# Kernel tuning notes

Measured on AMD Instinct MI355X. Metric: run time of the kernel, lower is better.

The kernel has to match this reference:

```python
import jax, jax.numpy as jnp
import numpy as np

B, S, H, L = 64, 512, 1024, 5  # batch, seq_len, BiLSTM feature dim (2*512), num fine P labels


def setup_inputs() -> dict:
    key = jax.random.key(0)
    ks = jax.random.split(key, 8)
    feats = jax.random.normal(ks[0], (B, S, H), dtype=jnp.float32)
    labels = jax.random.randint(ks[1], (B, S), 0, L)
    mask = jnp.ones((B, S), dtype=bool)  # CRF requires mask[:, 0] all on
    W_tag = jax.random.normal(ks[2], (H, L), dtype=jnp.float32) * 0.02
    b_tag = jnp.zeros((L,), dtype=jnp.float32)
    start_trans = jax.random.normal(ks[3], (L,), dtype=jnp.float32) * 0.1
    end_trans = jax.random.normal(ks[4], (L,), dtype=jnp.float32) * 0.1
    trans = jax.random.normal(ks[5], (L, L), dtype=jnp.float32) * 0.1
    weights = jax.random.uniform(ks[6], (L,), dtype=jnp.float32, minval=0.5, maxval=1.5)
    return dict(feats=feats, labels=labels, mask=mask, W_tag=W_tag, b_tag=b_tag,
                start_trans=start_trans, end_trans=end_trans, trans=trans, weights=weights)


def reference(feats, labels, mask, W_tag, b_tag, start_trans, end_trans, trans, weights):
    # hidden2tag + relu (as in the torch module: probablity = F.relu(self.hidden2tag(...)))
    emissions = jax.nn.relu(feats @ W_tag + b_tag)  # [B, S, L]
    maskf = mask.astype(emissions.dtype)            # [B, S]

    # ---- weighted CRF negative log-likelihood, reduction='token_mean' ----
    # numerator: gold-path score, per-token emission contributions scaled by class weights
    em_tag = jnp.take_along_axis(emissions, labels[..., None], axis=2)[..., 0]  # [B, S]
    numerator = (start_trans[labels[:, 0]]
                 + jnp.sum(weights[labels] * em_tag * maskf, axis=1)
                 + jnp.sum(trans[labels[:, :-1], labels[:, 1:]] * maskf[:, 1:], axis=1)
                 + end_trans[labels[:, -1]])  # [B]

    # partition function via forward algorithm (scan over time)
    emis_t = emissions[:, 1:].swapaxes(0, 1)  # [S-1, B, L]
    mask_t = mask[:, 1:].T                    # [S-1, B]

    def fwd_step(alpha, x):
        e, m = x  # [B, L], [B]
        new = jax.nn.logsumexp(alpha[:, :, None] + trans[None, :, :], axis=1) + e
        return jnp.where(m[:, None], new, alpha), None

    alpha0 = start_trans[None, :] + emissions[:, 0]  # [B, L]
    alpha, _ = jax.lax.scan(fwd_step, alpha0, (emis_t, mask_t))
    log_z = jax.nn.logsumexp(alpha + end_trans[None, :], axis=1)  # [B]

    loss = -jnp.sum(numerator - log_z) / maskf.sum()

    # ---- Viterbi decode ----
    def vit_step(v, x):
        e, m = x
        scores = v[:, :, None] + trans[None, :, :]  # [B, L_prev, L_cur]
        best = jnp.max(scores, axis=1) + e
        idx = jnp.argmax(scores, axis=1)            # backpointers [B, L]
        return jnp.where(m[:, None], best, v), idx

    v, hist = jax.lax.scan(vit_step, start_trans[None, :] + emissions[:, 0], (emis_t, mask_t))
    last = jnp.argmax(v + end_trans[None, :], axis=1)  # [B] tag at position S-1
    b_idx = jnp.arange(labels.shape[0])

    def back_step(tag, bp):
        prev = bp[b_idx, tag]
        return prev, tag  # emit tag at position t+1

    first, path_rest = jax.lax.scan(back_step, last, hist, reverse=True)  # [B], [S-1, B]
    paths = jnp.concatenate([first[None, :], path_rest], axis=0).T  # [B, S]

    return loss, paths
```

## Files before the change

kernel.cpp:

```cpp
#include <hip/hip_runtime.h>

namespace {

constexpr int kB = 64, kS = 512, kH = 1024, kL = 5;
constexpr int kRows = kB * kS;
constexpr float kNegInf = -1e30f;
constexpr int kChunks = 6;

__device__ inline float rl(float x, int i) {
  return __uint_as_float(__builtin_amdgcn_readlane(__float_as_uint(x), i));
}

__global__ __launch_bounds__(256) void emis_kernel(
    const float* __restrict__ feats, const float* __restrict__ W,
    const float* __restrict__ b_tag, float* __restrict__ emis,
    float* __restrict__ out_loss, int nwaves) {
  if (blockIdx.x == 0 && threadIdx.x == 0) out_loss[0] = 0.0f;

  const int lane = threadIdx.x & 63;
  const int wave = blockIdx.x * (blockDim.x >> 6) + (threadIdx.x >> 6);

  float wreg[4][20];
#pragma unroll
  for (int k0 = 0; k0 < 4; ++k0) {
    const float4* wp =
        reinterpret_cast<const float4*>(W + (k0 * 256 + lane * 4) * kL);
#pragma unroll
    for (int q = 0; q < 5; ++q) {
      float4 w = wp[q];
      wreg[k0][q * 4 + 0] = w.x;
      wreg[k0][q * 4 + 1] = w.y;
      wreg[k0][q * 4 + 2] = w.z;
      wreg[k0][q * 4 + 3] = w.w;
    }
  }

  for (int r = 2 * wave; r < kRows; r += 2 * nwaves) {
    const float4* fa = reinterpret_cast<const float4*>(feats + (size_t)r * kH);
    const float4* fb =
        reinterpret_cast<const float4*>(feats + (size_t)(r + 1) * kH);
    float accA[kL] = {0.f, 0.f, 0.f, 0.f, 0.f};
    float accB[kL] = {0.f, 0.f, 0.f, 0.f, 0.f};
#pragma unroll
    for (int k0 = 0; k0 < 4; ++k0) {
      float4 xa = fa[(k0 << 6) + lane];
      float4 xb = fb[(k0 << 6) + lane];
      const float* wr = wreg[k0];
#pragma unroll
      for (int l = 0; l < kL; ++l) {
        accA[l] = fmaf(xa.x, wr[l], accA[l]);
        accA[l] = fmaf(xa.y, wr[5 + l], accA[l]);
        accA[l] = fmaf(xa.z, wr[10 + l], accA[l]);
        accA[l] = fmaf(xa.w, wr[15 + l], accA[l]);
        accB[l] = fmaf(xb.x, wr[l], accB[l]);
        accB[l] = fmaf(xb.y, wr[5 + l], accB[l]);
        accB[l] = fmaf(xb.z, wr[10 + l], accB[l]);
        accB[l] = fmaf(xb.w, wr[15 + l], accB[l]);
      }
    }
#pragma unroll
    for (int off = 32; off >= 1; off >>= 1)
#pragma unroll
      for (int l = 0; l < kL; ++l) {
        accA[l] += __shfl_xor(accA[l], off, 64);
        accB[l] += __shfl_xor(accB[l], off, 64);
      }
    if (lane < kL) {
      emis[(size_t)r * kL + lane] = fmaxf(accA[lane] + b_tag[lane], 0.0f);
      emis[(size_t)(r + 1) * kL + lane] = fmaxf(accB[lane] + b_tag[lane], 0.0f);
    }
  }
}

__global__ __launch_bounds__(512) void scan_kernel(
    const float* __restrict__ emis, const int* __restrict__ labels,
    const float* __restrict__ start_trans, const float* __restrict__ end_trans,
    const float* __restrict__ trans, const float* __restrict__ weights,
    float* __restrict__ out_loss, float* __restrict__ out_paths) {
  const int b = blockIdx.x;
  const int tid = threadIdx.x;
  const int lane = tid & 63;
  const int wv = tid >> 6;

  __shared__ float e_lds[(kS + 4) * kL];
  __shared__ float v_lds[kS * kL];
  __shared__ float t_lds[25];
  __shared__ unsigned short f_a[kS], f_b[kS];
  __shared__ float M_lds[kChunks * 25];
  __shared__ double num_sh;
  __shared__ int last_sh;

  {
    const float4* src =
        reinterpret_cast<const float4*>(emis + (size_t)b * kS * kL);
    float4* dst = reinterpret_cast<float4*>(e_lds);
    for (int i = tid; i < kS * kL / 4; i += 512) dst[i] = src[i];
    if (tid < 4 * kL) e_lds[kS * kL + tid] = 0.0f;
    if (tid < 25) t_lds[tid] = trans[tid];
  }
  __syncthreads();

  const int j = (lane < kL) ? lane : 0;

  if (wv == 0) {
    const bool act = lane < kL;
    float tf[kL];
#pragma unroll
    for (int i = 0; i < kL; ++i) tf[i] = t_lds[i * kL + j];
    float vd = start_trans[j] + e_lds[j];
    if (act) v_lds[lane] = vd;
    float e0 = e_lds[1 * kL + j], e1 = e_lds[2 * kL + j],
          e2 = e_lds[3 * kL + j], e3 = e_lds[4 * kL + j];
#pragma unroll 4
    for (int t = 1; t < kS; ++t) {
      float en = e_lds[(t + 4) * kL + j];
      float s0 = rl(vd, 0), s1 = rl(vd, 1), s2 = rl(vd, 2), s3 = rl(vd, 3),
            s4 = rl(vd, 4);
      float c0 = s0 + tf[0], c1 = s1 + tf[1], c2 = s2 + tf[2],
            c3 = s3 + tf[3], c4 = s4 + tf[4];
      float m = fmaxf(fmaxf(fmaxf(c0, c1), fmaxf(c2, c3)), c4);
      vd = m + e0;
      if (act) v_lds[t * kL + lane] = vd;
      e0 = e1; e1 = e2; e2 = e3; e3 = en;
    }
    float v0 = rl(vd, 0), v1 = rl(vd, 1), v2 = rl(vd, 2), v3 = rl(vd, 3),
          v4 = rl(vd, 4);
    if (lane == 0) {
      float best = v0 + end_trans[0];
      int last = 0;
      float cc;
      cc = v1 + end_trans[1]; if (cc > best) { best = cc; last = 1; }
      cc = v2 + end_trans[2]; if (cc > best) { best = cc; last = 2; }
      cc = v3 + end_trans[3]; if (cc > best) { best = cc; last = 3; }
      cc = v4 + end_trans[4]; if (cc > best) { best = cc; last = 4; }
      last_sh = last;
    }
  } else if (wv == 1) {
    double num = 0.0;
    for (int t = lane; t < kS; t += 64) {
      int lt = labels[b * kS + t];
      num += (double)weights[lt] * (double)e_lds[t * kL + lt];
      if (t > 0) {
        int lp = labels[b * kS + t - 1];
        num += (double)t_lds[lp * kL + lt];
      }
    }
#pragma unroll
    for (int off = 32; off >= 1; off >>= 1) num += __shfl_xor(num, off, 64);
    if (lane == 0) {
      int l0 = labels[b * kS];
      int lS = labels[b * kS + kS - 1];
      num_sh = num + (double)start_trans[l0] + (double)end_trans[lS];
    }
  } else {
    const int c = wv - 2;
    const int t0 = 1 + 86 * c;
    const int t1 = (t0 + 86 < kS) ? (t0 + 86) : kS;
    const int ci = (lane < 25) ? (lane / 5) : 0;
    const int cj = (lane < 25) ? (lane % 5) : 0;
    float tf[kL];
#pragma unroll
    for (int k = 0; k < kL; ++k) tf[k] = t_lds[k * kL + cj];
    float m = (lane < 25 && ci == cj) ? 0.0f : kNegInf;
    float e_cur = e_lds[t0 * kL + cj];
    for (int t = t0; t < t1; ++t) {
      float e_nxt = (t + 1 < t1) ? e_lds[(t + 1) * kL + cj] : 0.0f;
      float m0 = __shfl(m, ci * 5 + 0, 64), m1 = __shfl(m, ci * 5 + 1, 64),
            m2 = __shfl(m, ci * 5 + 2, 64), m3 = __shfl(m, ci * 5 + 3, 64),
            m4 = __shfl(m, ci * 5 + 4, 64);
      float c0 = m0 + tf[0], c1 = m1 + tf[1], c2 = m2 + tf[2],
            c3 = m3 + tf[3], c4 = m4 + tf[4];
      float mx = fmaxf(fmaxf(fmaxf(c0, c1), fmaxf(c2, c3)), c4);
      float s = __expf(c0 - mx) + __expf(c1 - mx) + __expf(c2 - mx) +
                __expf(c3 - mx) + __expf(c4 - mx);
      m = mx + __logf(s) + e_cur;
      e_cur = e_nxt;
    }
    if (lane < 25) M_lds[c * 25 + lane] = m;
  }
  __syncthreads();

  if (tid < kS - 1) {
    float v0 = v_lds[tid * kL + 0], v1 = v_lds[tid * kL + 1],
          v2 = v_lds[tid * kL + 2], v3 = v_lds[tid * kL + 3],
          v4 = v_lds[tid * kL + 4];
    unsigned int w = 0;
#pragma unroll
    for (int q = 0; q < kL; ++q) {
      float best = v0 + t_lds[0 * kL + q];
      int bi = 0;
      float bb;
      bb = v1 + t_lds[1 * kL + q]; if (bb > best) { best = bb; bi = 1; }
      bb = v2 + t_lds[2 * kL + q]; if (bb > best) { best = bb; bi = 2; }
      bb = v3 + t_lds[3 * kL + q]; if (bb > best) { best = bb; bi = 3; }
      bb = v4 + t_lds[4 * kL + q]; if (bb > best) { best = bb; bi = 4; }
      w |= (unsigned int)bi << (3 * q);
    }
    f_a[tid + 1] = (unsigned short)w;
  }
  __syncthreads();

  unsigned short* src = f_a;
  unsigned short* dst = f_b;
  for (int off = 1; off < kS; off <<= 1) {
    if (tid >= 1) {
      unsigned short v = src[tid];
      if (tid + off < kS) {
        unsigned int a = v, g = src[tid + off], r = 0;
#pragma unroll
        for (int x = 0; x < kL; ++x) {
          unsigned int bx = (g >> (3 * x)) & 7u;
          r |= ((a >> (3 * bx)) & 7u) << (3 * x);
        }
        v = (unsigned short)r;
      }
      dst[tid] = v;
    }
    __syncthreads();
    unsigned short* tmp = src; src = dst; dst = tmp;
  }

  const int last = last_sh;
  if (tid < kS - 1) {
    unsigned short g = src[tid + 1];
    out_paths[(size_t)b * kS + tid] = (float)((g >> (3 * last)) & 7u);
  } else if (tid == kS - 1) {
    out_paths[(size_t)b * kS + tid] = (float)last;
  }

  if (wv == 1) {
    float alpha = start_trans[j] + e_lds[j];
#pragma unroll 1
    for (int c = 0; c < kChunks; ++c) {
      float a0 = __shfl(alpha, 0, 64), a1 = __shfl(alpha, 1, 64),
            a2 = __shfl(alpha, 2, 64), a3 = __shfl(alpha, 3, 64),
            a4 = __shfl(alpha, 4, 64);
      float c0 = a0 + M_lds[c * 25 + 0 + j], c1 = a1 + M_lds[c * 25 + 5 + j],
            c2 = a2 + M_lds[c * 25 + 10 + j], c3 = a3 + M_lds[c * 25 + 15 + j],
            c4 = a4 + M_lds[c * 25 + 20 + j];
      float mx = fmaxf(fmaxf(fmaxf(c0, c1), fmaxf(c2, c3)), c4);
      float s = __expf(c0 - mx) + __expf(c1 - mx) + __expf(c2 - mx) +
                __expf(c3 - mx) + __expf(c4 - mx);
      alpha = mx + __logf(s);
    }
    float aj[kL];
#pragma unroll
    for (int i = 0; i < kL; ++i) aj[i] = __shfl(alpha, i, 64);
    if (lane == 0) {
      float c0 = aj[0] + end_trans[0], c1 = aj[1] + end_trans[1],
            c2 = aj[2] + end_trans[2], c3 = aj[3] + end_trans[3],
            c4 = aj[4] + end_trans[4];
      float mx = fmaxf(fmaxf(fmaxf(c0, c1), fmaxf(c2, c3)), c4);
      float logz =
          mx + __logf(__expf(c0 - mx) + __expf(c1 - mx) + __expf(c2 - mx) +
                      __expf(c3 - mx) + __expf(c4 - mx));
      double term = num_sh - (double)logz;
      atomicAdd(out_loss, (float)(-term / (double)(kB * kS)));
    }
  }
}

}

extern "C" void kernel_launch(void* const* d_in, const int* in_sizes, int n_in,
                              void* d_out, int out_size, void* d_ws,
                              size_t ws_size, hipStream_t stream) {
  const float* feats = (const float*)d_in[0];
  const int* labels = (const int*)d_in[1];
  const float* W_tag = (const float*)d_in[3];
  const float* b_tag = (const float*)d_in[4];
  const float* start_trans = (const float*)d_in[5];
  const float* end_trans = (const float*)d_in[6];
  const float* trans = (const float*)d_in[7];
  const float* weights = (const float*)d_in[8];

  float* emis = (float*)d_ws;
  float* out = (float*)d_out;

  const int blocks = 2048;
  const int nwaves = blocks * 4;
  emis_kernel<<<blocks, 256, 0, stream>>>(feats, W_tag, b_tag, emis, out,
                                          nwaves);
  scan_kernel<<<kB, 512, 0, stream>>>(emis, labels, start_trans, end_trans,
                                      trans, weights, out, out + 1);
}
```

Baseline: 234.3 us.

## Fuse emission GEMV and CRF scan into one kernel with per-batch ready flags

Merges the emission projection and the CRF forward/Viterbi scan into a single launch. The emission blocks are assigned per batch, and each one increments that batch's flag after storing its rows. Scan blocks, placed at the end of the grid, spin on their batch's flag and start as soon as that batch's emissions are ready. This removes the kernel boundary and lets scans overlap the remaining GEMV work, at the cost of two memsets, atomic stores, and a forward-progress dependence on scan blocks being scheduled after the producer blocks.

```diff
diff --git a/kernel.cpp b/kernel.cpp
--- a/kernel.cpp
+++ b/kernel.cpp
@@ -3,39 +3,47 @@
 namespace {
 
 constexpr int kB = 64, kS = 512, kH = 1024, kL = 5;
-constexpr int kRows = kB * kS;
 constexpr float kNegInf = -1e30f;
 constexpr int kChunks = 6;
+constexpr int kEmisBlocks = 2048;
+constexpr int kBlocksPerBatch = 32;
 
 __device__ inline float rl(float x, int i) {
   return __uint_as_float(__builtin_amdgcn_readlane(__float_as_uint(x), i));
 }
 
-__global__ __launch_bounds__(256) void emis_kernel(
+__global__ __launch_bounds__(512) void fused_kernel(
     const float* __restrict__ feats, const float* __restrict__ W,
-    const float* __restrict__ b_tag, float* __restrict__ emis,
-    float* __restrict__ out_loss, int nwaves) {
-  if (blockIdx.x == 0 && threadIdx.x == 0) out_loss[0] = 0.0f;
-
-  const int lane = threadIdx.x & 63;
-  const int wave = blockIdx.x * (blockDim.x >> 6) + (threadIdx.x >> 6);
-
-  float wreg[4][20];
-#pragma unroll
-  for (int k0 = 0; k0 < 4; ++k0) {
-    const float4* wp =
-        reinterpret_cast<const float4*>(W + (k0 * 256 + lane * 4) * kL);
-#pragma unroll
-    for (int q = 0; q < 5; ++q) {
-      float4 w = wp[q];
-      wreg[k0][q * 4 + 0] = w.x;
-      wreg[k0][q * 4 + 1] = w.y;
-      wreg[k0][q * 4 + 2] = w.z;
-      wreg[k0][q * 4 + 3] = w.w;
-    }
-  }
-
-  for (int r = 2 * wave; r < kRows; r += 2 * nwaves) {
+    const float* __restrict__ b_tag, const int* __restrict__ labels,
+    const float* __restrict__ start_trans, const float* __restrict__ end_trans,
+    const float* __restrict__ trans, const float* __restrict__ weights,
+    float* __restrict__ emis, int* __restrict__ flags,
+    float* __restrict__ out_loss, float* __restrict__ out_paths) {
+  const int bidx = blockIdx.x;
+  const int tid = threadIdx.x;
+  const int lane = tid & 63;
+  const int wv = tid >> 6;
+
+  if (bidx < kEmisBlocks) {
+    const int batch = bidx / kBlocksPerBatch;
+    const int sub = bidx % kBlocksPerBatch;
+    const int r = batch * kS + sub * 16 + wv * 2;
+
+    float wreg[4][20];
+#pragma unroll
+    for (int k0 = 0; k0 < 4; ++k0) {
+      const float4* wp =
+          reinterpret_cast<const float4*>(W + (k0 * 256 + lane * 4) * kL);
+#pragma unroll
+      for (int q = 0; q < 5; ++q) {
+        float4 w = wp[q];
+        wreg[k0][q * 4 + 0] = w.x;
+        wreg[k0][q * 4 + 1] = w.y;
+        wreg[k0][q * 4 + 2] = w.z;
+        wreg[k0][q * 4 + 3] = w.w;
+      }
+    }
+
     const float4* fa = reinterpret_cast<const float4*>(feats + (size_t)r * kH);
     const float4* fb =
         reinterpret_cast<const float4*>(feats + (size_t)(r + 1) * kH);
@@ -66,21 +74,21 @@
         accB[l] += __shfl_xor(accB[l], off, 64);
       }
     if (lane < kL) {
-      emis[(size_t)r * kL + lane] = fmaxf(accA[lane] + b_tag[lane], 0.0f);
-      emis[(size_t)(r + 1) * kL + lane] = fmaxf(accB[lane] + b_tag[lane], 0.0f);
-    }
-  }
-}
-
-__global__ __launch_bounds__(512) void scan_kernel(
-    const float* __restrict__ emis, const int* __restrict__ labels,
-    const float* __restrict__ start_trans, const float* __restrict__ end_trans,
-    const float* __restrict__ trans, const float* __restrict__ weights,
-    float* __restrict__ out_loss, float* __restrict__ out_paths) {
-  const int b = blockIdx.x;
-  const int tid = threadIdx.x;
-  const int lane = tid & 63;
-  const int wv = tid >> 6;
+      __hip_atomic_store(&emis[(size_t)r * kL + lane],
+                         fmaxf(accA[lane] + b_tag[lane], 0.0f),
+                         __ATOMIC_RELAXED, __HIP_MEMORY_SCOPE_AGENT);
+      __hip_atomic_store(&emis[(size_t)(r + 1) * kL + lane],
+                         fmaxf(accB[lane] + b_tag[lane], 0.0f),
+                         __ATOMIC_RELAXED, __HIP_MEMORY_SCOPE_AGENT);
+    }
+    __syncthreads();
+    if (tid == 0)
+      __hip_atomic_fetch_add(&flags[batch], 1, __ATOMIC_RELEASE,
+                             __HIP_MEMORY_SCOPE_AGENT);
+    return;
+  }
+
+  const int b = bidx - kEmisBlocks;
 
   __shared__ float e_lds[(kS + 4) * kL];
   __shared__ float v_lds[kS * kL];
@@ -90,13 +98,22 @@
   __shared__ double num_sh;
   __shared__ int last_sh;
 
+  if (tid < 25) t_lds[tid] = trans[tid];
+  if (tid < 4 * kL) e_lds[kS * kL + tid] = 0.0f;
+
+  if (tid == 0) {
+    while (__hip_atomic_load(&flags[b], __ATOMIC_ACQUIRE,
+                             __HIP_MEMORY_SCOPE_AGENT) < kBlocksPerBatch) {
+      __builtin_amdgcn_s_sleep(1);
+    }
+  }
+  __syncthreads();
+
   {
     const float4* src =
         reinterpret_cast<const float4*>(emis + (size_t)b * kS * kL);
     float4* dst = reinterpret_cast<float4*>(e_lds);
     for (int i = tid; i < kS * kL / 4; i += 512) dst[i] = src[i];
-    if (tid < 4 * kL) e_lds[kS * kL + tid] = 0.0f;
-    if (tid < 25) t_lds[tid] = trans[tid];
   }
   __syncthreads();
 
@@ -274,13 +291,14 @@
   const float* trans = (const float*)d_in[7];
   const float* weights = (const float*)d_in[8];
 
-  float* emis = (float*)d_ws;
+  int* flags = (int*)d_ws;
+  float* emis = (float*)((char*)d_ws + 256);
   float* out = (float*)d_out;
 
-  const int blocks = 2048;
-  const int nwaves = blocks * 4;
-  emis_kernel<<<blocks, 256, 0, stream>>>(feats, W_tag, b_tag, emis, out,
-                                          nwaves);
-  scan_kernel<<<kB, 512, 0, stream>>>(emis, labels, start_trans, end_trans,
-                                      trans, weights, out, out + 1);
+  hipMemsetAsync(d_ws, 0, 256, stream);
+  hipMemsetAsync(d_out, 0, 4, stream);
+
+  fused_kernel<<<kEmisBlocks + kB, 512, 0, stream>>>(
+      feats, W_tag, b_tag, labels, start_trans, end_trans, trans, weights,
+      emis, flags, out, out + 1);
 }
```

Result: slower. 339.2 us (+44.7%).
